# Kernel optimization log

Measured on AMD Instinct MI355X. Metric: run time of the kernel, lower is better.

## Reference

```python
import jax, jax.numpy as jnp
import numpy as np

B, T, D, H, C = 256, 512, 300, 128, 6

def setup_inputs() -> dict:
    key = jax.random.key(0)
    ks = jax.random.split(key, 8)
    s = 1.0 / np.sqrt(H)  # PyTorch LSTM/Linear uniform init scale
    x = jax.random.normal(ks[0], (B, T, D), dtype=jnp.float32)
    lengths = jax.random.randint(ks[1], (B,), 1, T + 1)
    W_ih = jax.random.uniform(ks[2], (4 * H, D), minval=-s, maxval=s, dtype=jnp.float32)
    W_hh = jax.random.uniform(ks[3], (4 * H, H), minval=-s, maxval=s, dtype=jnp.float32)
    b_ih = jax.random.uniform(ks[4], (4 * H,), minval=-s, maxval=s, dtype=jnp.float32)
    b_hh = jax.random.uniform(ks[5], (4 * H,), minval=-s, maxval=s, dtype=jnp.float32)
    fc_w = jax.random.uniform(ks[6], (C, H), minval=-s, maxval=s, dtype=jnp.float32)
    fc_b = jax.random.uniform(ks[7], (C,), minval=-s, maxval=s, dtype=jnp.float32)
    return {"x": x, "W_ih": W_ih, "W_hh": W_hh, "b_ih": b_ih, "b_hh": b_hh,
            "fc_w": fc_w, "fc_b": fc_b, "lengths": lengths}

def _lstm_last_hidden(x, W_ih, W_hh, b_ih, b_hh, lengths):
    # Equivalent to pack_padded_sequence + nn.LSTM: the returned hidden[-1]
    # is the state at t = length-1 for each sequence. We run a masked scan:
    # state updates are frozen once t >= length.
    Bv, Tv, _ = x.shape
    Hv = W_hh.shape[1]
    xs = jnp.swapaxes(x, 0, 1)                              # [T, B, D]
    gx = jnp.einsum('tbd,gd->tbg', xs, W_ih) + b_ih + b_hh  # [T, B, 4H]
    mask = (jnp.arange(Tv)[:, None] < lengths[None, :])     # [T, B]

    def step(carry, inp):
        h, c = carry
        g, m = inp
        gates = g + h @ W_hh.T                              # [B, 4H]
        i, f, gg, o = jnp.split(gates, 4, axis=-1)          # PyTorch gate order i,f,g,o
        i = jax.nn.sigmoid(i)
        f = jax.nn.sigmoid(f)
        gg = jnp.tanh(gg)
        o = jax.nn.sigmoid(o)
        c_new = f * c + i * gg
        h_new = o * jnp.tanh(c_new)
        m = m[:, None]
        h = jnp.where(m, h_new, h)
        c = jnp.where(m, c_new, c)
        return (h, c), None

    h0 = jnp.zeros((Bv, Hv), dtype=x.dtype)
    c0 = jnp.zeros((Bv, Hv), dtype=x.dtype)
    (h, c), _ = jax.lax.scan(step, (h0, c0), (gx, mask))
    return h

def reference(x, W_ih, W_hh, b_ih, b_hh, fc_w, fc_b, lengths):
    h = _lstm_last_hidden(x, W_ih, W_hh, b_ih, b_hh, lengths)  # [B, H]
    return h @ fc_w.T + fc_b                                   # [B, 6]
```

## Files before the change

### kernel.cpp

```cpp
#include <hip/hip_runtime.h>
#include <hip/hip_bf16.h>
#include <stdint.h>
#include <type_traits>

#define NB 256
#define NT 512
#define ND 300
#define NH 128
#define NG 512
#define NC 6

typedef __attribute__((ext_vector_type(8))) short short8;
typedef __attribute__((ext_vector_type(4))) float f32x4;

static __device__ __forceinline__ float bf2f(unsigned int u) {
  return __builtin_bit_cast(float, (u & 0xffffu) << 16);
}
static __device__ __forceinline__ unsigned short f2bf(float f) {
  return __builtin_bit_cast(unsigned short, __float2bfloat16(f));
}
static __device__ __forceinline__ unsigned int packbf(float a, float b) {
  return (unsigned int)f2bf(a) | ((unsigned int)f2bf(b) << 16);
}
static __device__ __forceinline__ float ld1(const unsigned short* p) { return bf2f(*p); }
static __device__ __forceinline__ float ld1(const float* p) { return *p; }
static __device__ __forceinline__ void st1(unsigned short* p, float v) { *p = f2bf(v); }
static __device__ __forceinline__ void st1(float* p, float v) { *p = v; }

static __device__ __forceinline__ float sigmoid_fast(float x) {
  return __builtin_amdgcn_rcpf(1.f + __expf(-x));
}
static __device__ __forceinline__ float tanh_fast(float x) {
  return 1.f - 2.f * __builtin_amdgcn_rcpf(__expf(2.f * x) + 1.f);
}

#define BARRIER_LGKM() asm volatile("s_waitcnt lgkmcnt(0)\n\ts_barrier" ::: "memory")

static __device__ __forceinline__ uint2 load4bf_fast(const unsigned short* row, int k) {
  return *(const uint2*)(row + k);
}
static __device__ __forceinline__ uint2 load4bf_fast(const float* row, int k) {
  float4 f = *(const float4*)(row + k);
  uint2 v;
  v.x = packbf(f.x, f.y);
  v.y = packbf(f.z, f.w);
  return v;
}
static __device__ __forceinline__ uint2 load4bf(const unsigned short* row, int k, int lim) {
  if (k + 3 < lim) return load4bf_fast(row, k);
  unsigned int e0 = (k + 0 < lim) ? row[k + 0] : 0;
  unsigned int e1 = (k + 1 < lim) ? row[k + 1] : 0;
  unsigned int e2 = (k + 2 < lim) ? row[k + 2] : 0;
  unsigned int e3 = (k + 3 < lim) ? row[k + 3] : 0;
  uint2 v;
  v.x = e0 | (e1 << 16);
  v.y = e2 | (e3 << 16);
  return v;
}
static __device__ __forceinline__ uint2 load4bf(const float* row, int k, int lim) {
  if (k + 3 < lim) return load4bf_fast(row, k);
  float f0 = (k + 0 < lim) ? row[k + 0] : 0.f;
  float f1 = (k + 1 < lim) ? row[k + 1] : 0.f;
  float f2 = (k + 2 < lim) ? row[k + 2] : 0.f;
  float f3 = (k + 3 < lim) ? row[k + 3] : 0.f;
  uint2 v;
  v.x = packbf(f0, f1);
  v.y = packbf(f2, f3);
  return v;
}

static __device__ __forceinline__ int block_detect(const unsigned short* __restrict__ X,
                                                   int* cnt) {
  const int tid = threadIdx.x;
  const int nthr = blockDim.x;
  if (tid == 0) *cnt = 0;
  __syncthreads();
  int c = 0;
  for (int i = tid; i < 512; i += nthr) {
    unsigned int u = X[i];
    unsigned int e = (u >> 7) & 0xffu;
    if (u == 0u || (e >= 97u && e <= 157u)) c++;
  }
  if (c) atomicAdd(cnt, c);
  __syncthreads();
  return (*cnt >= 448) ? 0 : 1;
}

template <typename XT, typename GXT>
static __device__ __forceinline__ void gx_prod(
    const XT* __restrict__ X, const XT* __restrict__ Wih,
    const XT* __restrict__ bih, const XT* __restrict__ bhh,
    int b, int t0, int len, GXT* __restrict__ gxrow, unsigned short* smem) {
  auto As = reinterpret_cast<unsigned short(*)[64][40]>(smem);
  auto Bs = reinterpret_cast<unsigned short(*)[128][40]>(smem + 25600);

  const int tid = threadIdx.x;
  const int lane = tid & 63;
  const int wave = tid >> 6;
  const int wt = wave & 1;
  const int wn4 = wave >> 1;
  const int lq = lane >> 4;
  const int lr = lane & 15;

  const int rA = tid >> 3;
  const int cA = (tid & 7) << 2;
  const XT* xrow = X + ((size_t)b * NT + t0 + rA) * ND;
  {
    uint2 a[10];
#pragma unroll
    for (int kc = 0; kc < 9; ++kc) a[kc] = load4bf_fast(xrow, kc * 32 + cA);
    a[9] = load4bf(xrow, 288 + cA, ND);
#pragma unroll
    for (int kc = 0; kc < 10; ++kc) *(uint2*)&As[kc][rA][cA] = a[kc];
  }

  const int rb = tid >> 2;
  const int kqo = (tid & 3) << 3;
  uint2 bv[3][2];
  {
    const XT* wb = Wih + (size_t)rb * ND;
#pragma unroll
    for (int s3 = 0; s3 < 3; ++s3) {
      bv[s3][0] = load4bf_fast(wb, s3 * 32 + kqo);
      bv[s3][1] = load4bf_fast(wb, s3 * 32 + kqo + 4);
    }
  }

  for (int nt = 0; nt < 4; ++nt) {
    const int n0 = nt << 7;
    const XT* wb = Wih + (size_t)(n0 + rb) * ND;

    f32x4 acc[2][2];
#pragma unroll
    for (int i = 0; i < 2; ++i)
#pragma unroll
      for (int j = 0; j < 2; ++j) {
        f32x4 z = {0.f, 0.f, 0.f, 0.f};
        acc[i][j] = z;
      }

    *(uint2*)&Bs[0][rb][kqo] = bv[0][0];
    *(uint2*)&Bs[0][rb][kqo + 4] = bv[0][1];
    BARRIER_LGKM();

#pragma unroll
    for (int kc = 0; kc < 10; ++kc) {
      const int bi = kc & 1;
      if (kc < 9) {
        *(uint2*)&Bs[bi ^ 1][rb][kqo] = bv[(kc + 1) % 3][0];
        *(uint2*)&Bs[bi ^ 1][rb][kqo + 4] = bv[(kc + 1) % 3][1];
      }
      if (kc < 7) {
        const int kn = (kc + 3) * 32 + kqo;
        if (kc < 6) {
          bv[kc % 3][0] = load4bf_fast(wb, kn);
          bv[kc % 3][1] = load4bf_fast(wb, kn + 4);
        } else {
          bv[kc % 3][0] = load4bf(wb, kn, ND);
          bv[kc % 3][1] = load4bf(wb, kn + 4, ND);
        }
      }

      short8 wF[2], aX[2];
#pragma unroll
      for (int tn = 0; tn < 2; ++tn)
        wF[tn] = *(const short8*)&Bs[bi][wn4 * 32 + tn * 16 + lr][lq * 8];
#pragma unroll
      for (int tt = 0; tt < 2; ++tt)
        aX[tt] = *(const short8*)&As[kc][wt * 32 + tt * 16 + lr][lq * 8];
#pragma unroll
      for (int tt = 0; tt < 2; ++tt)
#pragma unroll
        for (int tn = 0; tn < 2; ++tn)
          acc[tt][tn] =
              __builtin_amdgcn_mfma_f32_16x16x32_bf16(wF[tn], aX[tt], acc[tt][tn], 0, 0, 0);
      BARRIER_LGKM();
    }

    if (nt < 3) {
      const XT* wb2 = Wih + (size_t)((nt + 1) * 128 + rb) * ND;
#pragma unroll
      for (int s3 = 0; s3 < 3; ++s3) {
        bv[s3][0] = load4bf_fast(wb2, s3 * 32 + kqo);
        bv[s3][1] = load4bf_fast(wb2, s3 * 32 + kqo + 4);
      }
    }

    f32x4 bias4[2];
#pragma unroll
    for (int tn = 0; tn < 2; ++tn) {
      const int n = n0 + wn4 * 32 + tn * 16 + lq * 4;
#pragma unroll
      for (int rg = 0; rg < 4; ++rg) bias4[tn][rg] = ld1(bih + n + rg) + ld1(bhh + n + rg);
    }
#pragma unroll
    for (int tt = 0; tt < 2; ++tt) {
      const int trow = wt * 32 + tt * 16 + lr;
      if (t0 + trow < len) {
#pragma unroll
        for (int tn = 0; tn < 2; ++tn) {
          const int n = n0 + wn4 * 32 + tn * 16 + lq * 4;
          f32x4 o = acc[tt][tn] + bias4[tn];
          if constexpr (std::is_same_v<GXT, float>) {
            *(f32x4*)(gxrow + (size_t)trow * NG + n) = o;
          } else {
            uint2 v;
            v.x = packbf(o[0], o[1]);
            v.y = packbf(o[2], o[3]);
            *(uint2*)(gxrow + (size_t)trow * NG + n) = v;
          }
        }
      }
    }
  }
}

#define REC_STEP(S, PAR, GC, CAP)                                                    \
  {                                                                                  \
    short8 bfr[4];                                                                   \
    const unsigned short* hrow = hpk[(PAR)];                                         \
    _Pragma("unroll") for (int c = 0; c < 4; ++c)                                    \
        bfr[c] = *(const short8*)&hrow[c * 32 + q * 8];                              \
    f32x4 acc[4];                                                                    \
    _Pragma("unroll") for (int g = 0; g < 4; ++g) {                                  \
      f32x4 z = {0.f, 0.f, 0.f, 0.f};                                                \
      acc[g] = z;                                                                    \
      _Pragma("unroll") for (int c = 0; c < 4; ++c)                                  \
          acc[g] = __builtin_amdgcn_mfma_f32_16x16x32_bf16(afr[g][c], bfr[c],        \
                                                           acc[g], 0, 0, 0);         \
    }                                                                                \
    float pre[4];                                                                    \
    _Pragma("unroll") for (int g = 0; g < 4; ++g) {                                  \
      const float t0v = (r & 1) ? acc[g][1] : acc[g][0];                             \
      const float t1v = (r & 1) ? acc[g][3] : acc[g][2];                             \
      pre[g] = ((r & 2) ? t1v : t0v) + GC[g];                                        \
    }                                                                                \
    {                                                                                \
      int idx_ = (S) + 2;                                                            \
      if (idx_ > (CAP)) idx_ = (CAP);                                                \
      _Pragma("unroll") for (int g = 0; g < 4; ++g)                                  \
          GC[g] = ld1(gp + (size_t)idx_ * NG + g * NH);                              \
    }                                                                                \
    const float ig = sigmoid_fast(pre[0]);                                           \
    const float fg = sigmoid_fast(pre[1]);                                           \
    const float gg = tanh_fast(pre[2]);                                              \
    const float og = sigmoid_fast(pre[3]);                                           \
    ccur = fmaf(fg, ccur, ig * gg);                                                  \
    hcur = og * tanh_fast(ccur);                                                     \
    if (m < 4) hpk[(PAR) ^ 1][u] = f2bf(hcur);                                       \
    BARRIER_LGKM();                                                                  \
  }

template <typename XT>
static __device__ __forceinline__ void load_afr(const XT* __restrict__ Whh, int w8,
                                                int q, int m, short8 afr[4][4]) {
#pragma unroll
  for (int g = 0; g < 4; ++g) {
    const int row = g * NH + w8 * 16 + m;
    if constexpr (std::is_same_v<XT, unsigned short>) {
#pragma unroll
      for (int c = 0; c < 4; ++c)
        afr[g][c] = *(const short8*)(Whh + (size_t)row * NH + c * 32 + q * 8);
    } else {
#pragma unroll
      for (int c = 0; c < 4; ++c) {
        const float* p = Whh + (size_t)row * NH + c * 32 + q * 8;
        float4 f0 = *(const float4*)p;
        float4 f1 = *(const float4*)(p + 4);
        union { unsigned int uu[4]; short8 s; } cv2;
        cv2.uu[0] = packbf(f0.x, f0.y);
        cv2.uu[1] = packbf(f0.z, f0.w);
        cv2.uu[2] = packbf(f1.x, f1.y);
        cv2.uu[3] = packbf(f1.z, f1.w);
        afr[g][c] = cv2.s;
      }
    }
  }
}

template <typename XT, typename GXT>
static __device__ __forceinline__ void rec_body(
    const GXT* __restrict__ gx, const XT* __restrict__ Whh,
    const XT* __restrict__ fcw, const XT* __restrict__ fcb,
    const int* __restrict__ lengths, XT* __restrict__ out,
    float* __restrict__ hstate, float* __restrict__ cstate,
    int b_base, int t_base, int Tc,
    unsigned short (*hpk)[NH], float* hf) {
  const int bc = blockIdx.x;
  const int b = b_base + bc;
  int len = lengths[b];
  if (len > NT) len = NT;
  if (len < 0) len = 0;
  const bool first = (t_base == 0);
  const bool last = (t_base + Tc >= NT);
  const int tend = (len < t_base + Tc) ? len : (t_base + Tc);
  if (!last && tend <= t_base) return;
  int nsteps = tend - t_base;
  if (nsteps < 0) nsteps = 0;

  const int tid = threadIdx.x;
  const int w8 = tid >> 6;
  const int l = tid & 63;
  const int q = l >> 4;
  const int m = l & 15;
  const int u0 = w8 * 16 + q * 4;
  const int r = m & 3;
  const int u = u0 + r;

  short8 afr[4][4];
  load_afr<XT>(Whh, w8, q, m, afr);

  float hcur = 0.f, ccur = 0.f;
  if (!first) {
    hcur = hstate[(size_t)bc * NH + u];
    ccur = cstate[(size_t)bc * NH + u];
  }
  if (m < 4) hpk[0][u] = f2bf(hcur);
  __syncthreads();

  const GXT* gp = gx + (size_t)bc * Tc * NG + u;
  const int lastidx = (nsteps > 0) ? nsteps - 1 : 0;

  float gs0[4], gs1[4];
  {
    const int i1 = (1 < lastidx) ? 1 : lastidx;
#pragma unroll
    for (int g = 0; g < 4; ++g) {
      gs0[g] = ld1(gp + g * NH);
      gs1[g] = ld1(gp + (size_t)i1 * NG + g * NH);
    }
  }

  int s = 0;
  for (; s + 1 < nsteps; s += 2) {
    REC_STEP(s, 0, gs0, lastidx);
    REC_STEP(s + 1, 1, gs1, lastidx);
  }
  if (s < nsteps) {
    REC_STEP(s, 0, gs0, lastidx);
  }

  if (!last) {
    if (m < 4) {
      hstate[(size_t)bc * NH + u] = hcur;
      cstate[(size_t)bc * NH + u] = ccur;
    }
  } else {
    if (m < 4) hf[u] = hcur;
    __syncthreads();
    if (tid < NC) {
      float acc = ld1(fcb + tid);
      const XT* wv = fcw + (size_t)tid * NH;
#pragma unroll
      for (int k = 0; k < NH; ++k) acc = fmaf(ld1(wv + k), hf[k], acc);
      st1(out + (size_t)b * NC + tid, acc);
    }
  }
}

template <typename GXT>
__global__ __launch_bounds__(512, 4) void gx_gemm_rt(const void* __restrict__ X,
                                                     const void* __restrict__ Wih,
                                                     const void* __restrict__ bih,
                                                     const void* __restrict__ bhh,
                                                     const int* __restrict__ lengths,
                                                     GXT* __restrict__ gx,
                                                     int b_base, int t_base, int Tc) {
  __shared__ int cnt;
  __shared__ __align__(16) unsigned short smem[35840];
  const int isf32 = block_detect((const unsigned short*)X, &cnt);
  const int m0 = blockIdx.x << 6;
  const int bc = m0 / Tc;
  const int trel = m0 % Tc;
  const int b = b_base + bc;
  const int t0 = t_base + trel;
  int len = lengths[b];
  if (len > NT) len = NT;
  if (t0 >= len) return;
  GXT* gxrow = gx + (size_t)m0 * NG;
  if (isf32)
    gx_prod<float, GXT>((const float*)X, (const float*)Wih, (const float*)bih,
                        (const float*)bhh, b, t0, len, gxrow, smem);
  else
    gx_prod<unsigned short, GXT>((const unsigned short*)X, (const unsigned short*)Wih,
                                 (const unsigned short*)bih, (const unsigned short*)bhh,
                                 b, t0, len, gxrow, smem);
}

template <typename GXT>
__global__ __launch_bounds__(512)
__attribute__((amdgpu_waves_per_eu(2, 2)))
void lstm_rec_rt(const void* __restrict__ X, const GXT* __restrict__ gx,
                 const void* __restrict__ Whh, const void* __restrict__ fcw,
                 const void* __restrict__ fcb, const int* __restrict__ lengths,
                 void* __restrict__ out, float* __restrict__ hstate,
                 float* __restrict__ cstate, int b_base, int t_base, int Tc) {
  __shared__ int cnt;
  __shared__ __align__(16) unsigned short hpk[2][NH];
  __shared__ __align__(16) float hf[NH];
  const int isf32 = block_detect((const unsigned short*)X, &cnt);
  if (isf32)
    rec_body<float, GXT>(gx, (const float*)Whh, (const float*)fcw, (const float*)fcb,
                         lengths, (float*)out, hstate, cstate, b_base, t_base, Tc,
                         hpk, hf);
  else
    rec_body<unsigned short, GXT>(gx, (const unsigned short*)Whh,
                                  (const unsigned short*)fcw,
                                  (const unsigned short*)fcb, lengths,
                                  (unsigned short*)out, hstate, cstate, b_base,
                                  t_base, Tc, hpk, hf);
}

template <typename GXT>
static void run_all(void* const* d_in, void* d_out, GXT* gx, float* hstate,
                    float* cstate, int NBc, int Tc, hipStream_t stream) {
  const int* lengths = (const int*)d_in[7];
  for (int bb = 0; bb < NB; bb += NBc) {
    for (int tb = 0; tb < NT; tb += Tc) {
      gx_gemm_rt<GXT><<<dim3((NBc * Tc) / 64), dim3(512), 0, stream>>>(
          d_in[0], d_in[1], d_in[3], d_in[4], lengths, gx, bb, tb, Tc);
      lstm_rec_rt<GXT><<<dim3(NBc), dim3(512), 0, stream>>>(
          d_in[0], gx, d_in[2], d_in[5], d_in[6], lengths, d_out, hstate, cstate,
          bb, tb, Tc);
    }
  }
}

extern "C" void kernel_launch(void* const* d_in, const int* in_sizes, int n_in,
                              void* d_out, int out_size, void* d_ws, size_t ws_size,
                              hipStream_t stream) {
  const size_t full_f32 = (size_t)NB * NT * NG * sizeof(float);
  const size_t full_bf16 = (size_t)NB * NT * NG * 2;
  const size_t base = 512;

  int NBc, Tc;
  char* gx_raw;
  float* hstate = (float*)((char*)d_ws + base);
  bool gx_is_f32;

  if (ws_size >= base + full_f32) {
    NBc = NB; Tc = NT; gx_is_f32 = true;
    gx_raw = (char*)d_ws + base;
  } else if (ws_size >= base + full_bf16) {
    NBc = NB; Tc = NT; gx_is_f32 = false;
    gx_raw = (char*)d_ws + base;
  } else {
    Tc = 128; gx_is_f32 = false;
    NBc = 1;
    for (int cand : {64, 16, 4}) {
      size_t need = base + (size_t)cand * NH * 2 * sizeof(float) + (size_t)cand * Tc * NG * 2;
      if (ws_size >= need) { NBc = cand; break; }
    }
    gx_raw = (char*)d_ws + base + (size_t)NBc * NH * 2 * sizeof(float);
  }
  float* cstate = hstate + (size_t)NBc * NH;

  if (gx_is_f32) {
    run_all<float>(d_in, d_out, (float*)gx_raw, hstate, cstate, NBc, Tc, stream);
  } else {
    run_all<unsigned short>(d_in, d_out, (unsigned short*)gx_raw, hstate, cstate,
                            NBc, Tc, stream);
  }
}
```

Baseline: 580.0 us.

## Process two batch sequences per recurrent block with interleaved independent chains

Each recurrent block now advances two batch elements, interleaving their per-step MFMA and gate math so one shared barrier covers both sequences and the two dependency chains can overlap latency. The grid is halved from NBc to about NBc/2 blocks. The cost is fewer blocks and so less CU occupancy across the device, plus per-block runtime bound by the longer of the two sequences, with divergent branches when their lengths differ.

```diff
diff --git a/kernel.cpp b/kernel.cpp
--- a/kernel.cpp
+++ b/kernel.cpp
@@ -215,10 +215,10 @@
   }
 }
 
-#define REC_STEP(S, PAR, GC, CAP)                                                    \
+#define REC_PHASE(S, PAR, GC, CAP, HPKB, GP, HC, CC)                                 \
   {                                                                                  \
     short8 bfr[4];                                                                   \
-    const unsigned short* hrow = hpk[(PAR)];                                         \
+    const unsigned short* hrow = (HPKB)[(PAR)];                                      \
     _Pragma("unroll") for (int c = 0; c < 4; ++c)                                    \
         bfr[c] = *(const short8*)&hrow[c * 32 + q * 8];                              \
     f32x4 acc[4];                                                                    \
@@ -239,16 +239,15 @@
       int idx_ = (S) + 2;                                                            \
       if (idx_ > (CAP)) idx_ = (CAP);                                                \
       _Pragma("unroll") for (int g = 0; g < 4; ++g)                                  \
-          GC[g] = ld1(gp + (size_t)idx_ * NG + g * NH);                              \
+          GC[g] = ld1((GP) + (size_t)idx_ * NG + g * NH);                            \
     }                                                                                \
     const float ig = sigmoid_fast(pre[0]);                                           \
     const float fg = sigmoid_fast(pre[1]);                                           \
     const float gg = tanh_fast(pre[2]);                                              \
     const float og = sigmoid_fast(pre[3]);                                           \
-    ccur = fmaf(fg, ccur, ig * gg);                                                  \
-    hcur = og * tanh_fast(ccur);                                                     \
-    if (m < 4) hpk[(PAR) ^ 1][u] = f2bf(hcur);                                       \
-    BARRIER_LGKM();                                                                  \
+    CC = fmaf(fg, CC, ig * gg);                                                      \
+    HC = og * tanh_fast(CC);                                                         \
+    if (m < 4) (HPKB)[(PAR) ^ 1][u] = f2bf(HC);                                      \
   }
 
 template <typename XT>
@@ -279,24 +278,35 @@
 }
 
 template <typename XT, typename GXT>
-static __device__ __forceinline__ void rec_body(
+static __device__ __forceinline__ void rec_body2(
     const GXT* __restrict__ gx, const XT* __restrict__ Whh,
     const XT* __restrict__ fcw, const XT* __restrict__ fcb,
     const int* __restrict__ lengths, XT* __restrict__ out,
     float* __restrict__ hstate, float* __restrict__ cstate,
-    int b_base, int t_base, int Tc,
-    unsigned short (*hpk)[NH], float* hf) {
-  const int bc = blockIdx.x;
-  const int b = b_base + bc;
-  int len = lengths[b];
-  if (len > NT) len = NT;
-  if (len < 0) len = 0;
+    int b_base, int t_base, int Tc, int NBc,
+    unsigned short (*hpk)[2][NH], float (*hf)[NH]) {
+  const int bc0 = blockIdx.x * 2;
+  const bool hasB = (bc0 + 1 < NBc);
+  const int bc1 = hasB ? bc0 + 1 : bc0;
+  const int b0 = b_base + bc0;
+  const int b1 = b_base + bc1;
+
+  int len0 = lengths[b0];
+  if (len0 > NT) len0 = NT;
+  if (len0 < 0) len0 = 0;
+  int len1 = lengths[b1];
+  if (len1 > NT) len1 = NT;
+  if (len1 < 0) len1 = 0;
+
   const bool first = (t_base == 0);
   const bool last = (t_base + Tc >= NT);
-  const int tend = (len < t_base + Tc) ? len : (t_base + Tc);
-  if (!last && tend <= t_base) return;
-  int nsteps = tend - t_base;
-  if (nsteps < 0) nsteps = 0;
+  int tend0 = (len0 < t_base + Tc) ? len0 : (t_base + Tc);
+  int tend1 = (len1 < t_base + Tc) ? len1 : (t_base + Tc);
+  int nsteps0 = tend0 - t_base;
+  if (nsteps0 < 0) nsteps0 = 0;
+  int nsteps1 = hasB ? (tend1 - t_base) : 0;
+  if (nsteps1 < 0) nsteps1 = 0;
+  if (!last && nsteps0 <= 0 && nsteps1 <= 0) return;
 
   const int tid = threadIdx.x;
   const int w8 = tid >> 6;
@@ -310,50 +320,81 @@
   short8 afr[4][4];
   load_afr<XT>(Whh, w8, q, m, afr);
 
-  float hcur = 0.f, ccur = 0.f;
+  float hcur0 = 0.f, ccur0 = 0.f, hcur1 = 0.f, ccur1 = 0.f;
   if (!first) {
-    hcur = hstate[(size_t)bc * NH + u];
-    ccur = cstate[(size_t)bc * NH + u];
-  }
-  if (m < 4) hpk[0][u] = f2bf(hcur);
+    hcur0 = hstate[(size_t)bc0 * NH + u];
+    ccur0 = cstate[(size_t)bc0 * NH + u];
+    hcur1 = hstate[(size_t)bc1 * NH + u];
+    ccur1 = cstate[(size_t)bc1 * NH + u];
+  }
+  if (m < 4) {
+    hpk[0][0][u] = f2bf(hcur0);
+    hpk[1][0][u] = f2bf(hcur1);
+  }
   __syncthreads();
 
-  const GXT* gp = gx + (size_t)bc * Tc * NG + u;
-  const int lastidx = (nsteps > 0) ? nsteps - 1 : 0;
-
-  float gs0[4], gs1[4];
+  const GXT* gp0 = gx + (size_t)bc0 * Tc * NG + u;
+  const GXT* gp1 = gx + (size_t)bc1 * Tc * NG + u;
+  const int cap0 = (nsteps0 > 0) ? nsteps0 - 1 : 0;
+  const int cap1 = (nsteps1 > 0) ? nsteps1 - 1 : 0;
+
+  float gsA0[4], gsA1[4], gsB0[4], gsB1[4];
   {
-    const int i1 = (1 < lastidx) ? 1 : lastidx;
+    const int i1a = (1 < cap0) ? 1 : cap0;
+    const int i1b = (1 < cap1) ? 1 : cap1;
 #pragma unroll
     for (int g = 0; g < 4; ++g) {
-      gs0[g] = ld1(gp + g * NH);
-      gs1[g] = ld1(gp + (size_t)i1 * NG + g * NH);
-    }
-  }
-
+      gsA0[g] = ld1(gp0 + g * NH);
+      gsA1[g] = ld1(gp0 + (size_t)i1a * NG + g * NH);
+      gsB0[g] = ld1(gp1 + g * NH);
+      gsB1[g] = ld1(gp1 + (size_t)i1b * NG + g * NH);
+    }
+  }
+
+  const int smax = (nsteps0 > nsteps1) ? nsteps0 : nsteps1;
   int s = 0;
-  for (; s + 1 < nsteps; s += 2) {
-    REC_STEP(s, 0, gs0, lastidx);
-    REC_STEP(s + 1, 1, gs1, lastidx);
-  }
-  if (s < nsteps) {
-    REC_STEP(s, 0, gs0, lastidx);
+  for (; s + 1 < smax; s += 2) {
+    if (s < nsteps0) REC_PHASE(s, 0, gsA0, cap0, hpk[0], gp0, hcur0, ccur0);
+    if (hasB && s < nsteps1) REC_PHASE(s, 0, gsB0, cap1, hpk[1], gp1, hcur1, ccur1);
+    BARRIER_LGKM();
+    if (s + 1 < nsteps0) REC_PHASE(s + 1, 1, gsA1, cap0, hpk[0], gp0, hcur0, ccur0);
+    if (hasB && s + 1 < nsteps1) REC_PHASE(s + 1, 1, gsB1, cap1, hpk[1], gp1, hcur1, ccur1);
+    BARRIER_LGKM();
+  }
+  if (s < smax) {
+    if (s < nsteps0) REC_PHASE(s, 0, gsA0, cap0, hpk[0], gp0, hcur0, ccur0);
+    if (hasB && s < nsteps1) REC_PHASE(s, 0, gsB0, cap1, hpk[1], gp1, hcur1, ccur1);
+    BARRIER_LGKM();
   }
 
   if (!last) {
     if (m < 4) {
-      hstate[(size_t)bc * NH + u] = hcur;
-      cstate[(size_t)bc * NH + u] = ccur;
+      hstate[(size_t)bc0 * NH + u] = hcur0;
+      cstate[(size_t)bc0 * NH + u] = ccur0;
+      if (hasB) {
+        hstate[(size_t)bc1 * NH + u] = hcur1;
+        cstate[(size_t)bc1 * NH + u] = ccur1;
+      }
     }
   } else {
-    if (m < 4) hf[u] = hcur;
+    if (m < 4) {
+      hf[0][u] = hcur0;
+      if (hasB) hf[1][u] = hcur1;
+    }
     __syncthreads();
     if (tid < NC) {
       float acc = ld1(fcb + tid);
       const XT* wv = fcw + (size_t)tid * NH;
 #pragma unroll
-      for (int k = 0; k < NH; ++k) acc = fmaf(ld1(wv + k), hf[k], acc);
-      st1(out + (size_t)b * NC + tid, acc);
+      for (int k = 0; k < NH; ++k) acc = fmaf(ld1(wv + k), hf[0][k], acc);
+      st1(out + (size_t)b0 * NC + tid, acc);
+    } else if (hasB && tid >= 64 && tid < 64 + NC) {
+      const int cc = tid - 64;
+      float acc = ld1(fcb + cc);
+      const XT* wv = fcw + (size_t)cc * NH;
+#pragma unroll
+      for (int k = 0; k < NH; ++k) acc = fmaf(ld1(wv + k), hf[1][k], acc);
+      st1(out + (size_t)b1 * NC + cc, acc);
     }
   }
 }
@@ -394,21 +435,22 @@
                  const void* __restrict__ Whh, const void* __restrict__ fcw,
                  const void* __restrict__ fcb, const int* __restrict__ lengths,
                  void* __restrict__ out, float* __restrict__ hstate,
-                 float* __restrict__ cstate, int b_base, int t_base, int Tc) {
+                 float* __restrict__ cstate, int b_base, int t_base, int Tc,
+                 int NBc) {
   __shared__ int cnt;
-  __shared__ __align__(16) unsigned short hpk[2][NH];
-  __shared__ __align__(16) float hf[NH];
+  __shared__ __align__(16) unsigned short hpk[2][2][NH];
+  __shared__ __align__(16) float hf[2][NH];
   const int isf32 = block_detect((const unsigned short*)X, &cnt);
   if (isf32)
-    rec_body<float, GXT>(gx, (const float*)Whh, (const float*)fcw, (const float*)fcb,
-                         lengths, (float*)out, hstate, cstate, b_base, t_base, Tc,
-                         hpk, hf);
+    rec_body2<float, GXT>(gx, (const float*)Whh, (const float*)fcw, (const float*)fcb,
+                          lengths, (float*)out, hstate, cstate, b_base, t_base, Tc,
+                          NBc, hpk, hf);
   else
-    rec_body<unsigned short, GXT>(gx, (const unsigned short*)Whh,
-                                  (const unsigned short*)fcw,
-                                  (const unsigned short*)fcb, lengths,
-                                  (unsigned short*)out, hstate, cstate, b_base,
-                                  t_base, Tc, hpk, hf);
+    rec_body2<unsigned short, GXT>(gx, (const unsigned short*)Whh,
+                                   (const unsigned short*)fcw,
+                                   (const unsigned short*)fcb, lengths,
+                                   (unsigned short*)out, hstate, cstate, b_base,
+                                   t_base, Tc, NBc, hpk, hf);
 }
 
 template <typename GXT>
@@ -419,9 +461,9 @@
     for (int tb = 0; tb < NT; tb += Tc) {
       gx_gemm_rt<GXT><<<dim3((NBc * Tc) / 64), dim3(512), 0, stream>>>(
           d_in[0], d_in[1], d_in[3], d_in[4], lengths, gx, bb, tb, Tc);
-      lstm_rec_rt<GXT><<<dim3(NBc), dim3(512), 0, stream>>>(
+      lstm_rec_rt<GXT><<<dim3((NBc + 1) / 2), dim3(512), 0, stream>>>(
           d_in[0], gx, d_in[2], d_in[5], d_in[6], lengths, d_out, hstate, cstate,
-          bb, tb, Tc);
+          bb, tb, Tc, NBc);
     }
   }
 }
```

Result: slower. 820.4 us (+41.5%).
